# Performance work log

Measured on AMD Instinct MI355X. Metric: run time of the kernel, lower is better.

## Reference

```python
import jax, jax.numpy as jnp
import numpy as np

IMG = 224
WS = 8      # windows_size
STRIDE = 2
M = 1

def _dct_mat(size):
    i = np.arange(size)[:, None]
    j = np.arange(size)[None, :]
    scale = np.where(i == 0, np.sqrt(1.0 / size), np.sqrt(2.0 / size))
    return (scale * np.cos((j + 0.5) * np.pi * i / size)).astype(np.float32)

def _gen_filter(start, end, size):
    i = np.arange(size)[:, None]
    j = np.arange(size)[None, :]
    s = i + j
    return np.where((s > end) | (s < start), 0.0, 1.0).astype(np.float32)

def setup_inputs() -> dict:
    key = jax.random.key(0)
    x = jax.random.normal(key, (16, 3, IMG, IMG), dtype=jnp.float32)
    D = jnp.asarray(_dct_mat(WS))                       # [ws, ws] DCT matrix
    filt = jnp.asarray(_gen_filter(WS // 3, WS * 2, WS))  # high-pass base filter
    return {"x": x, "D": D, "filt": filt}

def reference(x, D, filt):
    b, c, H, W = x.shape
    n = (H - WS) // STRIDE + 1                 # patches per side (109)
    rows = jnp.arange(n)[:, None] * STRIDE + jnp.arange(WS)[None, :]  # [n, ws]
    # unfold: overlapping stride-2 patches -> [b, n, n, c, ws, ws]
    p = x[:, :, rows, :]                       # [b, c, n, ws, W]
    p = p[..., rows]                           # [b, c, n, ws, n, ws]
    p = p.transpose(0, 2, 4, 1, 3, 5)          # [b, n, n, c, ws, ws]
    # block DCT: D @ p @ D^T
    xd = jnp.einsum('pi,bmncij,qj->bmncpq', D, p, D)
    # filter (use_learnable=False, norm=False -> plain elementwise mask)
    y = xd * filt
    # block IDCT: D^T @ y @ D
    y = jnp.einsum('pi,bmncpq,qj->bmncij', D, y, D)
    # fold: overlap-add scatter back to [b, c, H, W]
    hh = rows[:, None, :, None]                # [n,1,ws,1]
    ww = rows[None, :, None, :]                # [1,n,1,ws]
    flat = hh * W + ww                         # [n,n,ws,ws] flat spatial index
    y_t = y.transpose(0, 3, 1, 2, 4, 5)        # [b, c, n, n, ws, ws]
    out = jnp.zeros((b, c, H * W), x.dtype).at[:, :, flat].add(y_t)
    return out.reshape(b, c, H, W)             # m=1 -> cat is identity
```

## Files before the change

### kernel.cpp

```cpp
#include <hip/hip_runtime.h>

#define IMG 224
#define WS 8
#define STRIDE 2
#define NP 109
#define BC 48
#define NPIX (IMG * IMG)
#define NPATCH (NP * NP)
#define NQ 112
#define NQP (NQ * NQ)


#define LOAD_D_SCALARS(D)                                                  \
    const float d0_0 = (D)[0], d0_1 = (D)[1], d0_2 = (D)[2], d0_3 = (D)[3],\
                d0_4 = (D)[4], d0_5 = (D)[5], d0_6 = (D)[6], d0_7 = (D)[7];\
    const float d1_0 = (D)[8],  d1_1 = (D)[9],  d1_2 = (D)[10],            \
                d1_3 = (D)[11], d1_4 = (D)[12], d1_5 = (D)[13],            \
                d1_6 = (D)[14], d1_7 = (D)[15];

__global__ __launch_bounds__(256) void patch_coef_kernel(
    const float* __restrict__ x, const float* __restrict__ D,
    const float* __restrict__ filt,
    float2* __restrict__ cab, float* __restrict__ cc)
{
    int idx = blockIdx.x * blockDim.x + threadIdx.x;
    if (idx >= BC * NPATCH) return;
    int bc  = idx / NPATCH;
    int rem = idx - bc * NPATCH;
    int pr  = rem / NP;
    int pc  = rem - pr * NP;

    LOAD_D_SCALARS(D)

    const float* base = x + (size_t)bc * NPIX + (size_t)(pr * STRIDE) * IMG + (pc * STRIDE);
    float c00 = 0.f, c01 = 0.f, c10 = 0.f;

#define K1_ROW(i)                                                              \
    {                                                                          \
        const float2* row = (const float2*)(base + (size_t)(i) * IMG);         \
        float2 v0 = row[0], v1 = row[1], v2 = row[2], v3 = row[3];             \
        float s = fmaf(v0.x, d0_0, fmaf(v0.y, d0_1,                            \
                  fmaf(v1.x, d0_2, fmaf(v1.y, d0_3,                            \
                  fmaf(v2.x, d0_4, fmaf(v2.y, d0_5,                            \
                  fmaf(v3.x, d0_6, v3.y * d0_7)))))));                         \
        float t = fmaf(v0.x, d1_0, fmaf(v0.y, d1_1,                            \
                  fmaf(v1.x, d1_2, fmaf(v1.y, d1_3,                            \
                  fmaf(v2.x, d1_4, fmaf(v2.y, d1_5,                            \
                  fmaf(v3.x, d1_6, v3.y * d1_7)))))));                         \
        c00 = fmaf(d0_##i, s, c00);                                            \
        c01 = fmaf(d0_##i, t, c01);                                            \
        c10 = fmaf(d1_##i, s, c10);                                            \
    }

    K1_ROW(0) K1_ROW(1) K1_ROW(2) K1_ROW(3)
    K1_ROW(4) K1_ROW(5) K1_ROW(6) K1_ROW(7)
#undef K1_ROW

    float w00 = 1.0f - filt[0];
    float w01 = 1.0f - filt[1];
    float w10 = 1.0f - filt[8];
    cab[idx] = make_float2(c00 * w00, c01 * w01);
    cc[idx]  = c10 * w10;
}

__global__ __launch_bounds__(256) void gather2_kernel(
    const float* __restrict__ x, const float* __restrict__ D,
    const float2* __restrict__ cab, const float* __restrict__ cc,
    float* __restrict__ out)
{
    int idx = blockIdx.x * blockDim.x + threadIdx.x;
    if (idx >= BC * NQP) return;
    int bc  = idx / NQP;
    int rem = idx - bc * NQP;
    int qh  = rem / NQ;
    int qw  = rem - qh * NQ;

    LOAD_D_SCALARS(D)

    const float2* cabb = cab + (size_t)bc * NPATCH;
    const float*  ccb  = cc  + (size_t)bc * NPATCH;

    const int prb = qh - 3;
    const int pcb = qw - 3;

    float aee = 0.f, aeo = 0.f, aoe = 0.f, aoo = 0.f;

#define G_COL(kc, je, jo)                                                      \
    {                                                                          \
        int pc = pcb + (kc);                                                   \
        if (pc >= 0 && pc < NP) {                                              \
            int o = rowoff + pc;                                               \
            float2 ab = cabb[o];                                               \
            float  cv = ccb[o];                                                \
            Se = fmaf(ab.x, d0_##je, fmaf(ab.y, d1_##je, Se));                 \
            So = fmaf(ab.x, d0_##jo, fmaf(ab.y, d1_##jo, So));                 \
            Te = fmaf(cv, d0_##je, Te);                                        \
            To = fmaf(cv, d0_##jo, To);                                        \
        }                                                                      \
    }

#define G_ROW(kr, ie, io)                                                      \
    {                                                                          \
        int pr = prb + (kr);                                                   \
        if (pr >= 0 && pr < NP) {                                              \
            int rowoff = pr * NP;                                              \
            float Se = 0.f, So = 0.f, Te = 0.f, To = 0.f;                      \
            G_COL(0, 6, 7) G_COL(1, 4, 5) G_COL(2, 2, 3) G_COL(3, 0, 1)        \
            aee = fmaf(d0_##ie, Se, fmaf(d1_##ie, Te, aee));                   \
            aeo = fmaf(d0_##ie, So, fmaf(d1_##ie, To, aeo));                   \
            aoe = fmaf(d0_##io, Se, fmaf(d1_##io, Te, aoe));                   \
            aoo = fmaf(d0_##io, So, fmaf(d1_##io, To, aoo));                   \
        }                                                                      \
    }

    G_ROW(0, 6, 7) G_ROW(1, 4, 5) G_ROW(2, 2, 3) G_ROW(3, 0, 1)
#undef G_ROW
#undef G_COL

    int nvr = min(qh, NP - 1) - max(prb, 0) + 1;
    int nvc = min(qw, NP - 1) - max(pcb, 0) + 1;
    float cnt = (float)(nvr * nvc);

    int h0 = 2 * qh, w0 = 2 * qw;
    const float* xr = x   + (size_t)bc * NPIX + (size_t)h0 * IMG + w0;
    float*       orp = out + (size_t)bc * NPIX + (size_t)h0 * IMG + w0;
    float2 x0 = *(const float2*)xr;
    float2 x1 = *(const float2*)(xr + IMG);
    float2 o0, o1;
    o0.x = fmaf(cnt, x0.x, -aee);
    o0.y = fmaf(cnt, x0.y, -aeo);
    o1.x = fmaf(cnt, x1.x, -aoe);
    o1.y = fmaf(cnt, x1.y, -aoo);
    *(float2*)orp         = o0;
    *(float2*)(orp + IMG) = o1;
}

__global__ __launch_bounds__(256) void direct_kernel(
    const float* __restrict__ x, const float* __restrict__ D,
    const float* __restrict__ filt, float* __restrict__ out)
{
    int idx = blockIdx.x * blockDim.x + threadIdx.x;
    if (idx >= BC * NPIX) return;
    int bc  = idx / NPIX;
    int rem = idx - bc * NPIX;
    int h   = rem / IMG;
    int w   = rem - h * IMG;

    float D0[8], D1[8];
#pragma unroll
    for (int j = 0; j < 8; ++j) { D0[j] = D[j]; D1[j] = D[8 + j]; }
    float w00 = 1.0f - filt[0], w01 = 1.0f - filt[1], w10 = 1.0f - filt[8];

    int pr_lo = (h >= 6) ? ((h - 6) >> 1) : 0;
    int pr_hi = min(NP - 1, h >> 1);
    int pc_lo = (w >= 6) ? ((w - 6) >> 1) : 0;
    int pc_hi = min(NP - 1, w >> 1);

    const float* xbc = x + (size_t)bc * NPIX;
    float acc = 0.f;
    for (int pr = pr_lo; pr <= pr_hi; ++pr) {
        int i = h - STRIDE * pr;
        float d0i = D0[i], d1i = D1[i];
        for (int pc = pc_lo; pc <= pc_hi; ++pc) {
            int j = w - STRIDE * pc;
            const float* base = xbc + (size_t)(pr * STRIDE) * IMG + (pc * STRIDE);
            float c00 = 0.f, c01 = 0.f, c10 = 0.f;
            for (int ii = 0; ii < 8; ++ii) {
                float s = 0.f, t = 0.f;
                for (int jj = 0; jj < 8; ++jj) {
                    float v = base[(size_t)ii * IMG + jj];
                    s = fmaf(v, D0[jj], s);
                    t = fmaf(v, D1[jj], t);
                }
                c00 = fmaf(D0[ii], s, c00);
                c01 = fmaf(D0[ii], t, c01);
                c10 = fmaf(D1[ii], s, c10);
            }
            c00 *= w00; c01 *= w01; c10 *= w10;
            acc = fmaf(d0i, fmaf(c00, D0[j], c01 * D1[j]), fmaf(d1i, c10 * D0[j], acc));
        }
    }
    float cnt = (float)((pr_hi - pr_lo + 1) * (pc_hi - pc_lo + 1));
    out[idx] = cnt * x[idx] - acc;
}

extern "C" void kernel_launch(void* const* d_in, const int* in_sizes, int n_in,
                              void* d_out, int out_size, void* d_ws, size_t ws_size,
                              hipStream_t stream)
{
    const float* x    = (const float*)d_in[0];
    const float* D    = (const float*)d_in[1];
    const float* filt = (const float*)d_in[2];
    float* out        = (float*)d_out;

    const size_t plane = (size_t)BC * NPATCH;
    const size_t need  = plane * (sizeof(float2) + sizeof(float));

    if (ws_size >= need) {
        float2* cab = (float2*)d_ws;
        float*  cc  = (float*)(cab + plane);

        int npatch_tot = BC * NPATCH;
        patch_coef_kernel<<<(npatch_tot + 255) / 256, 256, 0, stream>>>(
            x, D, filt, cab, cc);

        int nquad_tot = BC * NQP;
        gather2_kernel<<<(nquad_tot + 255) / 256, 256, 0, stream>>>(
            x, D, cab, cc, out);
    } else {
        int npix_tot = BC * NPIX;
        direct_kernel<<<(npix_tot + 255) / 256, 256, 0, stream>>>(x, D, filt, out);
    }
}
```

Before: 83.19 us.

## Fuse patch coefficient and gather kernels into one shared-memory tiled kernel

```diff
diff --git a/kernel.cpp b/kernel.cpp
--- a/kernel.cpp
+++ b/kernel.cpp
@@ -1,14 +1,14 @@
 #include <hip/hip_runtime.h>
 
 #define IMG 224
-#define WS 8
-#define STRIDE 2
 #define NP 109
 #define BC 48
 #define NPIX (IMG * IMG)
-#define NPATCH (NP * NP)
-#define NQ 112
-#define NQP (NQ * NQ)
+#define TILE 56
+#define QT 28
+#define PT 31
+#define XR 68
+#define XC2 34
 
 
 #define LOAD_D_SCALARS(D)                                                  \
@@ -18,170 +18,129 @@
                 d1_3 = (D)[11], d1_4 = (D)[12], d1_5 = (D)[13],            \
                 d1_6 = (D)[14], d1_7 = (D)[15];
 
-__global__ __launch_bounds__(256) void patch_coef_kernel(
+__global__ __launch_bounds__(256) void fused_dct_kernel(
     const float* __restrict__ x, const float* __restrict__ D,
-    const float* __restrict__ filt,
-    float2* __restrict__ cab, float* __restrict__ cc)
+    const float* __restrict__ filt, float* __restrict__ out)
 {
-    int idx = blockIdx.x * blockDim.x + threadIdx.x;
-    if (idx >= BC * NPATCH) return;
-    int bc  = idx / NPATCH;
-    int rem = idx - bc * NPATCH;
-    int pr  = rem / NP;
-    int pc  = rem - pr * NP;
+    __shared__ float x_s[XR * XR];
+    __shared__ float ca_s[PT * PT];
+    __shared__ float cb_s[PT * PT];
+    __shared__ float cc_s[PT * PT];
+
+    const int tid = threadIdx.x;
+    const int h0 = blockIdx.y * TILE;
+    const int w0 = blockIdx.x * TILE;
+    const int bc = blockIdx.z;
 
     LOAD_D_SCALARS(D)
+    const float w00 = 1.0f - filt[0];
+    const float w01 = 1.0f - filt[1];
+    const float w10 = 1.0f - filt[8];
 
-    const float* base = x + (size_t)bc * NPIX + (size_t)(pr * STRIDE) * IMG + (pc * STRIDE);
-    float c00 = 0.f, c01 = 0.f, c10 = 0.f;
+    const float* xb = x + (size_t)bc * NPIX;
 
-#define K1_ROW(i)                                                              \
-    {                                                                          \
-        const float2* row = (const float2*)(base + (size_t)(i) * IMG);         \
-        float2 v0 = row[0], v1 = row[1], v2 = row[2], v3 = row[3];             \
-        float s = fmaf(v0.x, d0_0, fmaf(v0.y, d0_1,                            \
-                  fmaf(v1.x, d0_2, fmaf(v1.y, d0_3,                            \
-                  fmaf(v2.x, d0_4, fmaf(v2.y, d0_5,                            \
-                  fmaf(v3.x, d0_6, v3.y * d0_7)))))));                         \
-        float t = fmaf(v0.x, d1_0, fmaf(v0.y, d1_1,                            \
-                  fmaf(v1.x, d1_2, fmaf(v1.y, d1_3,                            \
-                  fmaf(v2.x, d1_4, fmaf(v2.y, d1_5,                            \
-                  fmaf(v3.x, d1_6, v3.y * d1_7)))))));                         \
-        c00 = fmaf(d0_##i, s, c00);                                            \
-        c01 = fmaf(d0_##i, t, c01);                                            \
-        c10 = fmaf(d1_##i, s, c10);                                            \
+    for (int i = tid; i < XR * XC2; i += 256) {
+        int r  = i / XC2;
+        int c2 = i - r * XC2;
+        int gr = h0 - 6 + r;
+        int gc = w0 - 6 + 2 * c2;
+        float2 v = make_float2(0.f, 0.f);
+        if ((unsigned)gr < (unsigned)IMG && (unsigned)gc < (unsigned)IMG)
+            v = *(const float2*)(xb + (size_t)gr * IMG + gc);
+        *(float2*)&x_s[r * XR + 2 * c2] = v;
     }
+    __syncthreads();
 
-    K1_ROW(0) K1_ROW(1) K1_ROW(2) K1_ROW(3)
-    K1_ROW(4) K1_ROW(5) K1_ROW(6) K1_ROW(7)
-#undef K1_ROW
+    const int pr0 = (h0 >> 1) - 3;
+    const int pc0 = (w0 >> 1) - 3;
+    for (int p = tid; p < PT * PT; p += 256) {
+        int prl = p / PT;
+        int pcl = p - prl * PT;
+        const float* wnd = &x_s[(2 * prl) * XR + 2 * pcl];
+        float c00 = 0.f, c01 = 0.f, c10 = 0.f;
 
-    float w00 = 1.0f - filt[0];
-    float w01 = 1.0f - filt[1];
-    float w10 = 1.0f - filt[8];
-    cab[idx] = make_float2(c00 * w00, c01 * w01);
-    cc[idx]  = c10 * w10;
-}
+#define C_ROW(i)                                                               \
+        {                                                                      \
+            const float2* prow = (const float2*)(wnd + (i) * XR);              \
+            float2 v0 = prow[0], v1 = prow[1], v2 = prow[2], v3 = prow[3];     \
+            float s = fmaf(v0.x, d0_0, fmaf(v0.y, d0_1,                        \
+                      fmaf(v1.x, d0_2, fmaf(v1.y, d0_3,                        \
+                      fmaf(v2.x, d0_4, fmaf(v2.y, d0_5,                        \
+                      fmaf(v3.x, d0_6, v3.y * d0_7)))))));                     \
+            float t = fmaf(v0.x, d1_0, fmaf(v0.y, d1_1,                        \
+                      fmaf(v1.x, d1_2, fmaf(v1.y, d1_3,                        \
+                      fmaf(v2.x, d1_4, fmaf(v2.y, d1_5,                        \
+                      fmaf(v3.x, d1_6, v3.y * d1_7)))))));                     \
+            c00 = fmaf(d0_##i, s, c00);                                        \
+            c01 = fmaf(d0_##i, t, c01);                                        \
+            c10 = fmaf(d1_##i, s, c10);                                        \
+        }
 
-__global__ __launch_bounds__(256) void gather2_kernel(
-    const float* __restrict__ x, const float* __restrict__ D,
-    const float2* __restrict__ cab, const float* __restrict__ cc,
-    float* __restrict__ out)
-{
-    int idx = blockIdx.x * blockDim.x + threadIdx.x;
-    if (idx >= BC * NQP) return;
-    int bc  = idx / NQP;
-    int rem = idx - bc * NQP;
-    int qh  = rem / NQ;
-    int qw  = rem - qh * NQ;
+        C_ROW(0) C_ROW(1) C_ROW(2) C_ROW(3)
+        C_ROW(4) C_ROW(5) C_ROW(6) C_ROW(7)
+#undef C_ROW
 
-    LOAD_D_SCALARS(D)
+        bool valid = ((unsigned)(pr0 + prl) < (unsigned)NP) &&
+                     ((unsigned)(pc0 + pcl) < (unsigned)NP);
+        float m = valid ? 1.0f : 0.0f;
+        ca_s[p] = c00 * w00 * m;
+        cb_s[p] = c01 * w01 * m;
+        cc_s[p] = c10 * w10 * m;
+    }
+    __syncthreads();
 
-    const float2* cabb = cab + (size_t)bc * NPATCH;
-    const float*  ccb  = cc  + (size_t)bc * NPATCH;
+    const int qh0 = h0 >> 1, qw0 = w0 >> 1;
+    float* ob = out + (size_t)bc * NPIX;
+    for (int q = tid; q < QT * QT; q += 256) {
+        int qhl = q / QT;
+        int qwl = q - qhl * QT;
 
-    const int prb = qh - 3;
-    const int pcb = qw - 3;
-
-    float aee = 0.f, aeo = 0.f, aoe = 0.f, aoo = 0.f;
+        float aee = 0.f, aeo = 0.f, aoe = 0.f, aoo = 0.f;
 
 #define G_COL(kc, je, jo)                                                      \
-    {                                                                          \
-        int pc = pcb + (kc);                                                   \
-        if (pc >= 0 && pc < NP) {                                              \
-            int o = rowoff + pc;                                               \
-            float2 ab = cabb[o];                                               \
-            float  cv = ccb[o];                                                \
-            Se = fmaf(ab.x, d0_##je, fmaf(ab.y, d1_##je, Se));                 \
-            So = fmaf(ab.x, d0_##jo, fmaf(ab.y, d1_##jo, So));                 \
-            Te = fmaf(cv, d0_##je, Te);                                        \
-            To = fmaf(cv, d0_##jo, To);                                        \
-        }                                                                      \
-    }
+        {                                                                      \
+            int o = ro + (kc);                                                 \
+            float a = ca_s[o], b = cb_s[o], c = cc_s[o];                       \
+            Se = fmaf(a, d0_##je, fmaf(b, d1_##je, Se));                       \
+            So = fmaf(a, d0_##jo, fmaf(b, d1_##jo, So));                       \
+            Te = fmaf(c, d0_##je, Te);                                         \
+            To = fmaf(c, d0_##jo, To);                                         \
+        }
 
 #define G_ROW(kr, ie, io)                                                      \
-    {                                                                          \
-        int pr = prb + (kr);                                                   \
-        if (pr >= 0 && pr < NP) {                                              \
-            int rowoff = pr * NP;                                              \
+        {                                                                      \
+            int ro = (qhl + (kr)) * PT + qwl;                                  \
             float Se = 0.f, So = 0.f, Te = 0.f, To = 0.f;                      \
             G_COL(0, 6, 7) G_COL(1, 4, 5) G_COL(2, 2, 3) G_COL(3, 0, 1)        \
             aee = fmaf(d0_##ie, Se, fmaf(d1_##ie, Te, aee));                   \
             aeo = fmaf(d0_##ie, So, fmaf(d1_##ie, To, aeo));                   \
             aoe = fmaf(d0_##io, Se, fmaf(d1_##io, Te, aoe));                   \
             aoo = fmaf(d0_##io, So, fmaf(d1_##io, To, aoo));                   \
-        }                                                                      \
-    }
+        }
 
-    G_ROW(0, 6, 7) G_ROW(1, 4, 5) G_ROW(2, 2, 3) G_ROW(3, 0, 1)
+        G_ROW(0, 6, 7) G_ROW(1, 4, 5) G_ROW(2, 2, 3) G_ROW(3, 0, 1)
 #undef G_ROW
 #undef G_COL
 
-    int nvr = min(qh, NP - 1) - max(prb, 0) + 1;
-    int nvc = min(qw, NP - 1) - max(pcb, 0) + 1;
-    float cnt = (float)(nvr * nvc);
+        int qh = qh0 + qhl, qw = qw0 + qwl;
+        int nvr = min(qh, NP - 1) - max(qh - 3, 0) + 1;
+        int nvc = min(qw, NP - 1) - max(qw - 3, 0) + 1;
+        float cnt = (float)(nvr * nvc);
 
-    int h0 = 2 * qh, w0 = 2 * qw;
-    const float* xr = x   + (size_t)bc * NPIX + (size_t)h0 * IMG + w0;
-    float*       orp = out + (size_t)bc * NPIX + (size_t)h0 * IMG + w0;
-    float2 x0 = *(const float2*)xr;
-    float2 x1 = *(const float2*)(xr + IMG);
-    float2 o0, o1;
-    o0.x = fmaf(cnt, x0.x, -aee);
-    o0.y = fmaf(cnt, x0.y, -aeo);
-    o1.x = fmaf(cnt, x1.x, -aoe);
-    o1.y = fmaf(cnt, x1.y, -aoo);
-    *(float2*)orp         = o0;
-    *(float2*)(orp + IMG) = o1;
-}
+        int lr = 2 * qhl + 6, lc = 2 * qwl + 6;
+        float2 x0 = *(const float2*)&x_s[lr * XR + lc];
+        float2 x1 = *(const float2*)&x_s[(lr + 1) * XR + lc];
 
-__global__ __launch_bounds__(256) void direct_kernel(
-    const float* __restrict__ x, const float* __restrict__ D,
-    const float* __restrict__ filt, float* __restrict__ out)
-{
-    int idx = blockIdx.x * blockDim.x + threadIdx.x;
-    if (idx >= BC * NPIX) return;
-    int bc  = idx / NPIX;
-    int rem = idx - bc * NPIX;
-    int h   = rem / IMG;
-    int w   = rem - h * IMG;
+        float2 o0, o1;
+        o0.x = fmaf(cnt, x0.x, -aee);
+        o0.y = fmaf(cnt, x0.y, -aeo);
+        o1.x = fmaf(cnt, x1.x, -aoe);
+        o1.y = fmaf(cnt, x1.y, -aoo);
 
-    float D0[8], D1[8];
-#pragma unroll
-    for (int j = 0; j < 8; ++j) { D0[j] = D[j]; D1[j] = D[8 + j]; }
-    float w00 = 1.0f - filt[0], w01 = 1.0f - filt[1], w10 = 1.0f - filt[8];
-
-    int pr_lo = (h >= 6) ? ((h - 6) >> 1) : 0;
-    int pr_hi = min(NP - 1, h >> 1);
-    int pc_lo = (w >= 6) ? ((w - 6) >> 1) : 0;
-    int pc_hi = min(NP - 1, w >> 1);
-
-    const float* xbc = x + (size_t)bc * NPIX;
-    float acc = 0.f;
-    for (int pr = pr_lo; pr <= pr_hi; ++pr) {
-        int i = h - STRIDE * pr;
-        float d0i = D0[i], d1i = D1[i];
-        for (int pc = pc_lo; pc <= pc_hi; ++pc) {
-            int j = w - STRIDE * pc;
-            const float* base = xbc + (size_t)(pr * STRIDE) * IMG + (pc * STRIDE);
-            float c00 = 0.f, c01 = 0.f, c10 = 0.f;
-            for (int ii = 0; ii < 8; ++ii) {
-                float s = 0.f, t = 0.f;
-                for (int jj = 0; jj < 8; ++jj) {
-                    float v = base[(size_t)ii * IMG + jj];
-                    s = fmaf(v, D0[jj], s);
-                    t = fmaf(v, D1[jj], t);
-                }
-                c00 = fmaf(D0[ii], s, c00);
-                c01 = fmaf(D0[ii], t, c01);
-                c10 = fmaf(D1[ii], s, c10);
-            }
-            c00 *= w00; c01 *= w01; c10 *= w10;
-            acc = fmaf(d0i, fmaf(c00, D0[j], c01 * D1[j]), fmaf(d1i, c10 * D0[j], acc));
-        }
+        float* orp = ob + (size_t)(h0 + 2 * qhl) * IMG + (w0 + 2 * qwl);
+        *(float2*)orp         = o0;
+        *(float2*)(orp + IMG) = o1;
     }
-    float cnt = (float)((pr_hi - pr_lo + 1) * (pc_hi - pc_lo + 1));
-    out[idx] = cnt * x[idx] - acc;
 }
 
 extern "C" void kernel_launch(void* const* d_in, const int* in_sizes, int n_in,
@@ -193,22 +152,7 @@
     const float* filt = (const float*)d_in[2];
     float* out        = (float*)d_out;
 
-    const size_t plane = (size_t)BC * NPATCH;
-    const size_t need  = plane * (sizeof(float2) + sizeof(float));
-
-    if (ws_size >= need) {
-        float2* cab = (float2*)d_ws;
-        float*  cc  = (float*)(cab + plane);
-
-        int npatch_tot = BC * NPATCH;
-        patch_coef_kernel<<<(npatch_tot + 255) / 256, 256, 0, stream>>>(
-            x, D, filt, cab, cc);
-
-        int nquad_tot = BC * NQP;
-        gather2_kernel<<<(nquad_tot + 255) / 256, 256, 0, stream>>>(
-            x, D, cab, cc, out);
-    } else {
-        int npix_tot = BC * NPIX;
-        direct_kernel<<<(npix_tot + 255) / 256, 256, 0, stream>>>(x, D, filt, out);
-    }
+    dim3 grid(IMG / TILE, IMG / TILE, BC);
+    fused_dct_kernel<<<grid, 256, 0, stream>>>(x, D, filt, out);
+    (void)d_ws; (void)ws_size;
 }
```

Result: faster. 77.51 us (-6.8%).
